# Kernel optimization log

Hardware: AMD Instinct MI355X
Metric: run time of the kernel (lower is better)

The kernel has to match this reference:

```python
import jax, jax.numpy as jnp
import numpy as np

K = 16
NS = [2048, 512, 128]

def _knn(q, r, k):
    # q: [B,M,3] query centers, r: [B,N,3] reference points -> (idx [B,M,k], sqdist [B,M,k])
    d2 = (jnp.sum(q * q, -1)[:, :, None] + jnp.sum(r * r, -1)[:, None, :]
          - 2.0 * jnp.einsum('bmd,bnd->bmn', q, r))
    neg, idx = jax.lax.top_k(-d2, k)
    return idx, jnp.maximum(-neg, 0.0)

def _gather(feat, idx):
    # feat [B,N,C], idx [B,M,k] -> [B,M,k,C]
    return jax.vmap(lambda f, i: f[i])(feat, idx)

def _down(x, pos, n, W1, b1, W2, b2):
    # PointNet++-style TransitionDown: sample n centers, kNN group, rel-pos concat, shared MLP, max-pool
    centers = pos[:, :n]
    idx, _ = _knn(centers, pos, K)
    rel = _gather(pos, idx) - centers[:, :, None, :]           # [B,n,K,3]
    feat = jnp.concatenate([rel, _gather(x, idx)], -1)          # [B,n,K,C+3]
    h = jax.nn.relu(feat @ W1 + b1) @ W2 + b2                   # last_act=False
    return jnp.max(h, axis=2), centers

def _up(xc, pc, prv_feat, prv_pos, W, b):
    # TransitionUp: 3-NN inverse-distance interpolation + skip concat + pointwise conv1d
    idx, d2 = _knn(prv_pos, pc, 3)
    w = 1.0 / (d2 + 1e-8)
    w = w / jnp.sum(w, -1, keepdims=True)
    interp = jnp.sum(_gather(xc, idx) * w[..., None], axis=2)   # [B,Nprv,Cc]
    cat = jnp.concatenate([interp, prv_feat], -1)
    return jax.nn.relu(cat @ W + b)

def setup_inputs() -> dict:
    key = jax.random.key(0)
    ks = jax.random.split(key, 16)
    p = lambda k, s: jax.random.normal(k, s, jnp.float32) * 0.02
    B, N = 4, 8192
    return {
        'x': jax.random.normal(ks[0], (B, N, 3), jnp.float32),
        'pos': jax.random.uniform(ks[1], (B, N, 3), jnp.float32),
        'd0_W1': p(ks[2], (6, 128)),   'd0_b1': jnp.zeros((128,), jnp.float32),
        'd0_W2': p(ks[3], (128, 128)), 'd0_b2': jnp.zeros((128,), jnp.float32),
        'd1_W1': p(ks[4], (131, 256)), 'd1_b1': jnp.zeros((256,), jnp.float32),
        'd1_W2': p(ks[5], (256, 256)), 'd1_b2': jnp.zeros((256,), jnp.float32),
        'd2_W1': p(ks[6], (259, 512)), 'd2_b1': jnp.zeros((512,), jnp.float32),
        'd2_W2': p(ks[7], (512, 512)), 'd2_b2': jnp.zeros((512,), jnp.float32),
        'u0_W': p(ks[8], (768, 256)),  'u0_b': jnp.zeros((256,), jnp.float32),
        'u1_W': p(ks[9], (384, 128)),  'u1_b': jnp.zeros((128,), jnp.float32),
        'u2_W': p(ks[10], (134, 128)), 'u2_b': jnp.zeros((128,), jnp.float32),
        'f_W1': p(ks[11], (128, 128)), 'f_b1': jnp.zeros((128,), jnp.float32),
        'f_W2': p(ks[12], (128, 128)), 'f_b2': jnp.zeros((128,), jnp.float32),
    }

def reference(x, pos, d0_W1, d0_b1, d0_W2, d0_b2, d1_W1, d1_b1, d1_W2, d1_b2,
              d2_W1, d2_b1, d2_W2, d2_b2, u0_W, u0_b, u1_W, u1_b, u2_W, u2_b,
              f_W1, f_b1, f_W2, f_b2):
    pos0, x0 = pos, x
    # encoder (transition-down) with cached (pos, x) per scale
    x1, pos1 = _down(x0, pos0, NS[0], d0_W1, d0_b1, d0_W2, d0_b2)
    x2, pos2 = _down(x1, pos1, NS[1], d1_W1, d1_b1, d1_W2, d1_b2)
    x3, pos3 = _down(x2, pos2, NS[2], d2_W1, d2_b1, d2_W2, d2_b2)
    # decoder (transition-up) consuming the cache in reverse; last level concats raw pos to skip feat
    up = _up(x3, pos3, x2, pos2, u0_W, u0_b)
    up = _up(up, pos2, x1, pos1, u1_W, u1_b)
    prv0 = jnp.concatenate([x0, pos0], -1)
    up = _up(up, pos1, prv0, pos0, u2_W, u2_b)
    # feat_map_layer_out: two pointwise conv1d layers, last_act=False
    out = jax.nn.relu(up @ f_W1 + f_b1) @ f_W2 + f_b2
    return (out, pos0)
```

## Files before the change

kernel.cpp:

```cpp
#include <hip/hip_runtime.h>

#define NFULL 8192
#define BATCH 4

typedef unsigned long long u64;
typedef unsigned int u32;
typedef __attribute__((ext_vector_type(8))) short bf8_t;
typedef __attribute__((ext_vector_type(4))) float f4_t;

__device__ __forceinline__ u32 fbias(float f) {
  u32 u = __float_as_uint(f);
  return (u & 0x80000000u) ? ~u : (u | 0x80000000u);
}
__device__ __forceinline__ float funbias(u32 b) {
  u32 u = (b & 0x80000000u) ? (b & 0x7fffffffu) : ~b;
  return __uint_as_float(u);
}
__device__ __forceinline__ short f2bf(float f) {
  u32 u = __float_as_uint(f);
  u32 r = u + 0x7FFFu + ((u >> 16) & 1u);
  return (short)(r >> 16);
}

__global__ __launch_bounds__(256) void build_grids_kernel(
    const float* __restrict__ pos, float4* __restrict__ sortedA,
    int* __restrict__ csA, float4* __restrict__ sortedB, int* __restrict__ csB,
    float4* __restrict__ sortedC, int* __restrict__ csC) {
  __shared__ int cnt[4096];
  __shared__ int partial[256];
  int which = blockIdx.y, b = blockIdx.x, t = threadIdx.x;
  int NREF = (which == 0) ? 8192 : (which == 1) ? 2048 : 512;
  int GR = (which == 0) ? 16 : 8;
  int NC = GR * GR * GR;
  float4* sorted = ((which == 0) ? sortedA : (which == 1) ? sortedB : sortedC)
                   + (size_t)b * NREF;
  int* cs = ((which == 0) ? csA + b * 4097 : (which == 1) ? csB + b * 513
                                           : csC + b * 513);
  const float* pb = pos + (size_t)b * NFULL * 3;
  for (int c = t; c < NC; c += 256) cnt[c] = 0;
  __syncthreads();
  for (int p = t; p < NREF; p += 256) {
    float x = pb[p * 3 + 0], y = pb[p * 3 + 1], z = pb[p * 3 + 2];
    int cx = min(max((int)(x * GR), 0), GR - 1);
    int cy = min(max((int)(y * GR), 0), GR - 1);
    int cz = min(max((int)(z * GR), 0), GR - 1);
    atomicAdd(&cnt[(cz * GR + cy) * GR + cx], 1);
  }
  __syncthreads();
  int chunk = (NC + 255) / 256;
  int s = 0;
  for (int i = 0; i < chunk; ++i) {
    int c = t * chunk + i;
    if (c < NC) s += cnt[c];
  }
  partial[t] = s;
  __syncthreads();
  if (t == 0) {
    int run = 0;
    for (int i = 0; i < 256; ++i) { int v = partial[i]; partial[i] = run; run += v; }
  }
  __syncthreads();
  int run = partial[t];
  for (int i = 0; i < chunk; ++i) {
    int c = t * chunk + i;
    if (c < NC) { int v = cnt[c]; cnt[c] = run; run += v; }
  }
  __syncthreads();
  for (int c = t; c < NC; c += 256) cs[c] = cnt[c];
  if (t == 0) cs[NC] = NREF;
  __syncthreads();
  for (int p = t; p < NREF; p += 256) {
    float x = pb[p * 3 + 0], y = pb[p * 3 + 1], z = pb[p * 3 + 2];
    int cx = min(max((int)(x * GR), 0), GR - 1);
    int cy = min(max((int)(y * GR), 0), GR - 1);
    int cz = min(max((int)(z * GR), 0), GR - 1);
    int slot = atomicAdd(&cnt[(cz * GR + cy) * GR + cx], 1);
    sorted[slot] = make_float4(x, y, z, __uint_as_float((u32)p));
  }
}

template<int SL>
__device__ __forceinline__ void group_insert(u32 m16, u64 ck, int slot,
                                             u64& val, u64& tau) {
  if (m16) {
    while (m16) {
      int src = __ffs(m16) - 1;
      m16 &= m16 - 1;
      u64 c = __shfl((unsigned long long)ck, src, 16);
      u64 prev = __shfl_up((unsigned long long)val, 1, SL);
      if (slot == 0) prev = 0ull;
      val = (val <= c) ? val : ((prev <= c) ? c : prev);
    }
    tau = __shfl((unsigned long long)val, SL - 1, SL);
  }
}

template<int SL>
__device__ __forceinline__ void first_round_sort(u64 ck, int gl,
                                                 u64& val, u64& tau) {
  u64 v = ck;
#pragma unroll
  for (int size = 2; size <= 16; size <<= 1) {
#pragma unroll
    for (int stride = size >> 1; stride > 0; stride >>= 1) {
      u64 other = __shfl_xor((unsigned long long)v, stride, 16);
      bool ddd = ((gl & size) == 0);
      bool takeMin = (((gl & stride) == 0) == ddd);
      u64 mn = (v <= other) ? v : other;
      u64 mx = (v <= other) ? other : v;
      v = takeMin ? mn : mx;
    }
  }
  if (SL < 16) v = __shfl((unsigned long long)v, gl & (SL - 1), 16);
  val = v;
  tau = __shfl((unsigned long long)v, SL - 1, SL);
}

template<int SL>
__device__ __forceinline__ void scan_range(const float4* __restrict__ sb,
    int s, int e, float qx, float qy, float qz, float qq,
    int g, int gl, int slot, u64& val, u64& tau) {
  for (int t0 = s; t0 < e; t0 += 16) {
    int j = t0 + gl;
    u64 ck = ~0ull;
    if (j < e) {
      float4 P = sb[j];
      float rr = P.x * P.x + P.y * P.y + P.z * P.z;
      float d2 = qq + rr - 2.0f * (qx * P.x + qy * P.y + qz * P.z);
      ck = ((u64)fbias(d2) << 32) | (u32)__float_as_uint(P.w);
    }
    u64 full = __ballot(ck < tau);
    u32 m16 = (u32)((full >> (g * 16)) & 0xFFFFull);
    group_insert<SL>(m16, ck, slot, val, tau);
  }
}


template<int SL, int KOUT, int GR, int R, int NREF>
__device__ __forceinline__ void knn_tail(
    const float4* __restrict__ sb, const int* __restrict__ cs,
    float qx, float qy, float qz, float qq,
    int ix, int iy, int iz, int x0, int x1, int y0, int y1, int z0, int z1,
    int g, int gl, int slot, u64& val, u64& tau) {
  const float h = 1.0f / GR;
  float m = 1e30f;
  if (x0 > 0)      m = fminf(m, qx - x0 * h);
  if (x1 < GR - 1) m = fminf(m, (x1 + 1) * h - qx);
  if (y0 > 0)      m = fminf(m, qy - y0 * h);
  if (y1 < GR - 1) m = fminf(m, (y1 + 1) * h - qy);
  if (z0 > 0)      m = fminf(m, qz - z0 * h);
  if (z1 < GR - 1) m = fminf(m, (z1 + 1) * h - qz);
  float bound = m * m;
  u64 kv = __shfl((unsigned long long)val, KOUT - 1, SL);
  float kth_d2 = funbias((u32)(kv >> 32));
  if (!(kth_d2 < bound)) {
    int X0 = max(ix - (R + 1), 0), X1 = min(ix + (R + 1), GR - 1);
    int Y0 = max(iy - (R + 1), 0), Y1 = min(iy + (R + 1), GR - 1);
    int Z0 = max(iz - (R + 1), 0), Z1 = min(iz + (R + 1), GR - 1);
    int NY2 = Y1 - Y0 + 1;
    int nrow2 = (Z1 - Z0 + 1) * NY2;
    for (int rr2 = 0; rr2 < nrow2; ++rr2) {
      int zz = Z0 + rr2 / NY2, yy = Y0 + rr2 % NY2;
      int c0 = (zz * GR + yy) * GR;
      bool mid = (zz >= z0 && zz <= z1 && yy >= y0 && yy <= y1);
      int s1 = cs[c0 + X0];
      int e1 = mid ? cs[c0 + x0] : cs[c0 + X1 + 1];
      scan_range<SL>(sb, s1, e1, qx, qy, qz, qq, g, gl, slot, val, tau);
      if (mid) {
        int s2 = cs[c0 + x1 + 1];
        int e2 = cs[c0 + X1 + 1];
        scan_range<SL>(sb, s2, e2, qx, qy, qz, qq, g, gl, slot, val, tau);
      }
    }
    x0 = X0; x1 = X1; y0 = Y0; y1 = Y1; z0 = Z0; z1 = Z1;
    m = 1e30f;
    if (x0 > 0)      m = fminf(m, qx - x0 * h);
    if (x1 < GR - 1) m = fminf(m, (x1 + 1) * h - qx);
    if (y0 > 0)      m = fminf(m, qy - y0 * h);
    if (y1 < GR - 1) m = fminf(m, (y1 + 1) * h - qy);
    if (z0 > 0)      m = fminf(m, qz - z0 * h);
    if (z1 < GR - 1) m = fminf(m, (z1 + 1) * h - qz);
    bound = m * m;
    kv = __shfl((unsigned long long)val, KOUT - 1, SL);
    kth_d2 = funbias((u32)(kv >> 32));
    if (!(kth_d2 < bound)) {
      for (int t0 = 0; t0 < NREF; t0 += 16) {
        int j = t0 + gl;
        u64 ck = ~0ull;
        if (j < NREF) {
          float4 P = sb[j];
          int cx = min(max((int)(P.x * GR), 0), GR - 1);
          int cy = min(max((int)(P.y * GR), 0), GR - 1);
          int cz = min(max((int)(P.z * GR), 0), GR - 1);
          bool inbox = (cx >= x0 && cx <= x1 && cy >= y0 && cy <= y1 &&
                        cz >= z0 && cz <= z1);
          if (!inbox) {
            float rr = P.x * P.x + P.y * P.y + P.z * P.z;
            float d2 = qq + rr - 2.0f * (qx * P.x + qy * P.y + qz * P.z);
            ck = ((u64)fbias(d2) << 32) | (u32)__float_as_uint(P.w);
          }
        }
        u64 full = __ballot(ck < tau);
        u32 m16 = (u32)((full >> (g * 16)) & 0xFFFFull);
        group_insert<SL>(m16, ck, slot, val, tau);
      }
    }
  }
}

template<int SL, int KOUT, int GR, int R, int NREF>
__device__ void knn_grid_flat_dev(int vbx,
    const float* __restrict__ pos, const float4* __restrict__ sorted,
    const int* __restrict__ cellStart, int csStride, int Mq,
    int* __restrict__ oidx, float* __restrict__ od2) {
  int b = blockIdx.y;
  int wv = threadIdx.x >> 6, lane = threadIdx.x & 63;
  int g = lane >> 4, gl = lane & 15;
  int q = vbx * 16 + wv * 4 + g;
  const float* pb = pos + (size_t)b * NFULL * 3;
  const float4* sb = sorted + (size_t)b * NREF;
  const int* cs = cellStart + b * csStride;
  float qx = pb[q * 3 + 0], qy = pb[q * 3 + 1], qz = pb[q * 3 + 2];
  float qq = qx * qx + qy * qy + qz * qz;
  int ix = min(max((int)(qx * GR), 0), GR - 1);
  int iy = min(max((int)(qy * GR), 0), GR - 1);
  int iz = min(max((int)(qz * GR), 0), GR - 1);
  int x0 = max(ix - R, 0), x1 = min(ix + R, GR - 1);
  int y0 = max(iy - R, 0), y1 = min(iy + R, GR - 1);
  int z0 = max(iz - R, 0), z1 = min(iz + R, GR - 1);

  int ny = y1 - y0 + 1;
  int nrow = (z1 - z0 + 1) * ny;
  int s_i = 0, len_i = 0;
  if (gl < nrow) {
    int zz = z0 + gl / ny, yy = y0 + gl % ny;
    int c0 = (zz * GR + yy) * GR + x0;
    s_i = cs[c0];
    len_i = cs[c0 + (x1 - x0) + 1] - s_i;
  }
  int p_i = len_i;
#pragma unroll
  for (int st = 1; st < 16; st <<= 1) {
    int o = __shfl_up(p_i, st, 16);
    if (gl >= st) p_i += o;
  }
  int T = __shfl(p_i, 15, 16);
  p_i -= len_i;
  int d_i = s_i - p_i;
  if (gl >= nrow) p_i = 0x7fffffff;

  int slot = gl & (SL - 1);
  u64 val, tau;

  {
    int v = gl;
    int r = 0;
#pragma unroll
    for (int st = 8; st >= 1; st >>= 1) {
      int pc = __shfl(p_i, r + st, 16);
      if (v >= pc) r += st;
    }
    int addr = v + __shfl(d_i, r, 16);
    u64 ck = ~0ull;
    if (v < T) {
      float4 P = sb[addr];
      float rr = P.x * P.x + P.y * P.y + P.z * P.z;
      float d2 = qq + rr - 2.0f * (qx * P.x + qy * P.y + qz * P.z);
      ck = ((u64)fbias(d2) << 32) | (u32)__float_as_uint(P.w);
    }
    first_round_sort<SL>(ck, gl, val, tau);
  }

  for (int v0 = 16; v0 < T; v0 += 16) {
    int v = v0 + gl;
    int r = 0;
#pragma unroll
    for (int st = 8; st >= 1; st >>= 1) {
      int pc = __shfl(p_i, r + st, 16);
      if (v >= pc) r += st;
    }
    int addr = v + __shfl(d_i, r, 16);
    u64 ck = ~0ull;
    if (v < T) {
      float4 P = sb[addr];
      float rr = P.x * P.x + P.y * P.y + P.z * P.z;
      float d2 = qq + rr - 2.0f * (qx * P.x + qy * P.y + qz * P.z);
      ck = ((u64)fbias(d2) << 32) | (u32)__float_as_uint(P.w);
    }
    u64 full = __ballot(ck < tau);
    u32 m16 = (u32)((full >> (g * 16)) & 0xFFFFull);
    group_insert<SL>(m16, ck, slot, val, tau);
  }

  knn_tail<SL, KOUT, GR, R, NREF>(sb, cs, qx, qy, qz, qq,
      ix, iy, iz, x0, x1, y0, y1, z0, z1, g, gl, slot, val, tau);

  if (gl < KOUT) {
    size_t base = ((size_t)b * Mq + q) * KOUT;
    oidx[base + gl] = (int)(u32)val;
    if (od2) od2[base + gl] = fmaxf(funbias((u32)(val >> 32)), 0.0f);
  }
}

template<int SL, int KOUT, int GR, int R, int NREF>
__device__ void knn_grid_flat32_dev(int vbx,
    const float* __restrict__ pos, const float4* __restrict__ sorted,
    const int* __restrict__ cellStart, int csStride, int Mq,
    int* __restrict__ oidx, float* __restrict__ od2) {
  int b = blockIdx.y;
  int wv = threadIdx.x >> 6, lane = threadIdx.x & 63;
  int g = lane >> 4, gl = lane & 15;
  int q = vbx * 16 + wv * 4 + g;
  const float* pb = pos + (size_t)b * NFULL * 3;
  const float4* sb = sorted + (size_t)b * NREF;
  const int* cs = cellStart + b * csStride;
  float qx = pb[q * 3 + 0], qy = pb[q * 3 + 1], qz = pb[q * 3 + 2];
  float qq = qx * qx + qy * qy + qz * qz;
  int ix = min(max((int)(qx * GR), 0), GR - 1);
  int iy = min(max((int)(qy * GR), 0), GR - 1);
  int iz = min(max((int)(qz * GR), 0), GR - 1);
  int x0 = max(ix - R, 0), x1 = min(ix + R, GR - 1);
  int y0 = max(iy - R, 0), y1 = min(iy + R, GR - 1);
  int z0 = max(iz - R, 0), z1 = min(iz + R, GR - 1);

  int ny = y1 - y0 + 1;
  int nrow = (z1 - z0 + 1) * ny;
  int sLo = 0, lenLo = 0, sHi = 0, lenHi = 0;
  if (gl < nrow) {
    int zz = z0 + gl / ny, yy = y0 + gl % ny;
    int c0 = (zz * GR + yy) * GR + x0;
    sLo = cs[c0]; lenLo = cs[c0 + (x1 - x0) + 1] - sLo;
  }
  {
    int i2 = gl + 16;
    if (i2 < nrow) {
      int zz = z0 + i2 / ny, yy = y0 + i2 % ny;
      int c0 = (zz * GR + yy) * GR + x0;
      sHi = cs[c0]; lenHi = cs[c0 + (x1 - x0) + 1] - sHi;
    }
  }
  int pLo = lenLo, pHi = lenHi;
#pragma unroll
  for (int st = 1; st < 16; st <<= 1) {
    int o = __shfl_up(pLo, st, 16);
    if (gl >= st) pLo += o;
    int o2 = __shfl_up(pHi, st, 16);
    if (gl >= st) pHi += o2;
  }
  int tot16 = __shfl(pLo, 15, 16);
  pHi += tot16;
  int T = __shfl(pHi, 15, 16);
  pLo -= lenLo; pHi -= lenHi;
  int dLo = sLo - pLo, dHi = sHi - pHi;
  if (gl >= nrow) pLo = 0x7fffffff;
  if (gl + 16 >= nrow) pHi = 0x7fffffff;

  int slot = gl & (SL - 1);
  u64 val, tau;

  {
    int v = gl;
    int r = 0;
#pragma unroll
    for (int st = 16; st >= 1; st >>= 1) {
      int j = r + st;
      int pcL = __shfl(pLo, j & 15, 16);
      int pcH = __shfl(pHi, j & 15, 16);
      int pc = (j < 16) ? pcL : pcH;
      if (v >= pc) r = j;
    }
    int dL = __shfl(dLo, r & 15, 16);
    int dH = __shfl(dHi, r & 15, 16);
    int addr = v + ((r < 16) ? dL : dH);
    u64 ck = ~0ull;
    if (v < T) {
      float4 P = sb[addr];
      float rr = P.x * P.x + P.y * P.y + P.z * P.z;
      float d2 = qq + rr - 2.0f * (qx * P.x + qy * P.y + qz * P.z);
      ck = ((u64)fbias(d2) << 32) | (u32)__float_as_uint(P.w);
    }
    first_round_sort<SL>(ck, gl, val, tau);
  }

  for (int v0 = 16; v0 < T; v0 += 16) {
    int v = v0 + gl;
    int r = 0;
#pragma unroll
    for (int st = 16; st >= 1; st >>= 1) {
      int j = r + st;
      int pcL = __shfl(pLo, j & 15, 16);
      int pcH = __shfl(pHi, j & 15, 16);
      int pc = (j < 16) ? pcL : pcH;
      if (v >= pc) r = j;
    }
    int dL = __shfl(dLo, r & 15, 16);
    int dH = __shfl(dHi, r & 15, 16);
    int addr = v + ((r < 16) ? dL : dH);
    u64 ck = ~0ull;
    if (v < T) {
      float4 P = sb[addr];
      float rr = P.x * P.x + P.y * P.y + P.z * P.z;
      float d2 = qq + rr - 2.0f * (qx * P.x + qy * P.y + qz * P.z);
      ck = ((u64)fbias(d2) << 32) | (u32)__float_as_uint(P.w);
    }
    u64 full = __ballot(ck < tau);
    u32 m16 = (u32)((full >> (g * 16)) & 0xFFFFull);
    group_insert<SL>(m16, ck, slot, val, tau);
  }

  knn_tail<SL, KOUT, GR, R, NREF>(sb, cs, qx, qy, qz, qq,
      ix, iy, iz, x0, x1, y0, y1, z0, z1, g, gl, slot, val, tau);

  if (gl < KOUT) {
    size_t base = ((size_t)b * Mq + q) * KOUT;
    oidx[base + gl] = (int)(u32)val;
    if (od2) od2[base + gl] = fmaxf(funbias((u32)(val >> 32)), 0.0f);
  }
}

template<int SL, int KOUT>
__device__ void knn_brute_dev(int vbx,
    const float* __restrict__ pos, int Nref, int Mq,
    int* __restrict__ oidx, float* __restrict__ od2) {
  int b = blockIdx.y;
  int wv = threadIdx.x >> 6, lane = threadIdx.x & 63;
  int g = lane >> 4, gl = lane & 15;
  int q = vbx * 16 + wv * 4 + g;
  const float* pb = pos + (size_t)b * NFULL * 3;
  float qx = pb[q * 3 + 0], qy = pb[q * 3 + 1], qz = pb[q * 3 + 2];
  float qq = qx * qx + qy * qy + qz * qz;

  int slot = gl & (SL - 1);
  u64 val, tau;

  {
    int j = gl;
    float rx = pb[j * 3 + 0];
    float ry = pb[j * 3 + 1];
    float rz = pb[j * 3 + 2];
    float rr = rx * rx + ry * ry + rz * rz;
    float d2 = qq + rr - 2.0f * (qx * rx + qy * ry + qz * rz);
    u64 ck = ((u64)fbias(d2) << 32) | (u32)j;
    first_round_sort<SL>(ck, gl, val, tau);
  }

  for (int t0 = 16; t0 < Nref; t0 += 16) {
    int j = t0 + gl;
    float rx = pb[j * 3 + 0];
    float ry = pb[j * 3 + 1];
    float rz = pb[j * 3 + 2];
    float rr = rx * rx + ry * ry + rz * rz;
    float d2 = qq + rr - 2.0f * (qx * rx + qy * ry + qz * rz);
    u64 ck = ((u64)fbias(d2) << 32) | (u32)j;
    u64 full = __ballot(ck < tau);
    u32 m16 = (u32)((full >> (g * 16)) & 0xFFFFull);
    group_insert<SL>(m16, ck, slot, val, tau);
  }

  if (gl < KOUT) {
    size_t base = ((size_t)b * Mq + q) * KOUT;
    oidx[base + gl] = (int)(u32)val;
    if (od2) od2[base + gl] = fmaxf(funbias((u32)(val >> 32)), 0.0f);
  }
}

__global__ __launch_bounds__(256) void knn_all_kernel(
    const float* __restrict__ pos,
    const float4* __restrict__ sortedA, const int* __restrict__ csA,
    const float4* __restrict__ sortedB, const int* __restrict__ csB,
    const float4* __restrict__ sortedC, const int* __restrict__ csC,
    int* __restrict__ idx0, int* __restrict__ idx1, int* __restrict__ idx2,
    int* __restrict__ idxu0, float* __restrict__ d2u0,
    int* __restrict__ idxu1, float* __restrict__ d2u1,
    int* __restrict__ idxu2, float* __restrict__ d2u2) {
  int bx = blockIdx.x;
  if (bx < 8)
    knn_brute_dev<16, 16>(bx, pos, 512, 128, idx2, nullptr);
  else if (bx < 40)
    knn_grid_flat32_dev<16, 16, 8, 2, 2048>(bx - 8, pos, sortedB, csB, 513, 512, idx1, nullptr);
  else if (bx < 168)
    knn_grid_flat32_dev<16, 16, 16, 2, 8192>(bx - 40, pos, sortedA, csA, 4097, 2048, idx0, nullptr);
  else if (bx < 296)
    knn_grid_flat32_dev<4, 3, 8, 2, 512>(bx - 168, pos, sortedC, csC, 513, 2048, idxu1, d2u1);
  else if (bx < 808)
    knn_grid_flat_dev<4, 3, 8, 1, 2048>(bx - 296, pos, sortedB, csB, 513, 8192, idxu2, d2u2);
  else
    knn_brute_dev<4, 3>(bx - 808, pos, 128, 512, idxu0, d2u0);
}

__device__ __forceinline__ void pack_tile_rt(const float* __restrict__ W,
                                             short* __restrict__ outp,
                                             int KDIM, int N, int tile, int lane) {
  int NT = N >> 4;
  int kt = tile / NT, nt = tile - kt * NT;
  int n = nt * 16 + (lane & 15);
  int k0 = kt * 32 + (lane >> 4) * 8;
  bf8_t v;
#pragma unroll
  for (int j = 0; j < 8; ++j) {
    int k = k0 + j;
    v[j] = (k < KDIM) ? f2bf(W[(size_t)k * N + n]) : (short)0;
  }
  *(bf8_t*)(outp + ((size_t)tile * 64 + lane) * 8) = v;
}

__global__ __launch_bounds__(64) void pack_copy_all_kernel(
    const float* d0W1, short* d0W1p, const float* d0W2, short* d0W2p,
    const float* d1W1, short* d1W1p, const float* d1W2, short* d1W2p,
    const float* d2W1, short* d2W1p, const float* d2W2, short* d2W2p,
    const float* u2W, short* u2Wp, const float* fW1, short* fW1p,
    const float* fW2, short* fW2p,
    const float* u0W, short* u0Wp, const float* u1W, short* u1Wp,
    const float* pos, float* posOut) {
  int blk = blockIdx.x, lane = threadIdx.x;
  if      (blk < 8)    pack_tile_rt(d0W1, d0W1p, 6, 128, blk, lane);
  else if (blk < 40)   pack_tile_rt(d0W2, d0W2p, 128, 128, blk - 8, lane);
  else if (blk < 120)  pack_tile_rt(d1W1, d1W1p, 131, 256, blk - 40, lane);
  else if (blk < 248)  pack_tile_rt(d1W2, d1W2p, 256, 256, blk - 120, lane);
  else if (blk < 536)  pack_tile_rt(d2W1, d2W1p, 259, 512, blk - 248, lane);
  else if (blk < 1048) pack_tile_rt(d2W2, d2W2p, 512, 512, blk - 536, lane);
  else if (blk < 1088) pack_tile_rt(u2W, u2Wp, 134, 128, blk - 1048, lane);
  else if (blk < 1120) pack_tile_rt(fW1, fW1p, 128, 128, blk - 1088, lane);
  else if (blk < 1152) pack_tile_rt(fW2, fW2p, 128, 128, blk - 1120, lane);
  else if (blk < 1536) pack_tile_rt(u0W, u0Wp, 768, 256, blk - 1152, lane);
  else if (blk < 1632) pack_tile_rt(u1W, u1Wp, 384, 128, blk - 1536, lane);
  else {
    int base = (blk - 1632) * 256;
#pragma unroll
    for (int j = 0; j < 4; ++j) {
      int i = base + lane + j * 64;
      posOut[i] = pos[i];
    }
  }
}

template<int FEAT, int CIN, int CHID, int FPAD, int QB, int WAVES>
__global__ __launch_bounds__(64 * WAVES) void down_mfma_kernel(
    const float* __restrict__ pos, const float* __restrict__ xin,
    const int* __restrict__ idx,
    const short* __restrict__ W1p, const float* __restrict__ b1,
    const short* __restrict__ W2p, const float* __restrict__ b2,
    float* __restrict__ out, int n, int nprev) {
  const int KT1 = FPAD / 32, NT1 = CHID / 16;
  const int KT2 = CHID / 32, NT2 = CHID / 16;
  __shared__ short sFeat[QB][16][FPAD + 8];
  __shared__ short sH1[QB][16][CHID + 8];
  __shared__ int sIdx[QB][16];
  __shared__ float sCtr[QB][3];
  int b = blockIdx.y, q0 = blockIdx.x * QB;
  int t = threadIdx.x;
  int lane = t & 63, wv = t >> 6;
  const float* pb = pos + (size_t)b * NFULL * 3;
  const float* xb = xin + (size_t)b * nprev * CIN;
  if (t < QB * 16)
    sIdx[t >> 4][t & 15] = idx[((size_t)b * n + q0 + (t >> 4)) * 16 + (t & 15)];
  if (t < QB * 3) sCtr[t / 3][t % 3] = pb[(q0 + t / 3) * 3 + (t % 3)];
  __syncthreads();
  for (int e = t; e < QB * 16 * FPAD; e += 64 * WAVES) {
    int k = e / FPAD, c = e - k * FPAD;
    int qq = k >> 4, kk = k & 15;
    float v = 0.f;
    if (c < 3) v = pb[sIdx[qq][kk] * 3 + c] - sCtr[qq][c];
    else if (c < FEAT) v = xb[(size_t)sIdx[qq][kk] * CIN + (c - 3)];
    sFeat[qq][kk][c] = f2bf(v);
  }
  __syncthreads();

  int col = lane & 15, quad = lane >> 4;
  const bf8_t* W1t = (const bf8_t*)W1p;
  for (int nt = 2 * wv; nt < NT1; nt += 2 * WAVES) {
    f4_t acc[QB][2];
    float bb0 = b1[nt * 16 + col], bb1 = b1[nt * 16 + 16 + col];
#pragma unroll
    for (int q = 0; q < QB; ++q) {
      acc[q][0] = {bb0, bb0, bb0, bb0};
      acc[q][1] = {bb1, bb1, bb1, bb1};
    }
#pragma unroll
    for (int kt = 0; kt < KT1; ++kt) {
      bf8_t bf0 = W1t[(kt * NT1 + nt) * 64 + lane];
      bf8_t bf1 = W1t[(kt * NT1 + nt + 1) * 64 + lane];
#pragma unroll
      for (int q = 0; q < QB; ++q) {
        bf8_t a = *(const bf8_t*)&sFeat[q][col][kt * 32 + quad * 8];
        acc[q][0] = __builtin_amdgcn_mfma_f32_16x16x32_bf16(a, bf0, acc[q][0], 0, 0, 0);
        acc[q][1] = __builtin_amdgcn_mfma_f32_16x16x32_bf16(a, bf1, acc[q][1], 0, 0, 0);
      }
    }
#pragma unroll
    for (int q = 0; q < QB; ++q)
#pragma unroll
      for (int r = 0; r < 4; ++r) {
        sH1[q][quad * 4 + r][nt * 16 + col] = f2bf(fmaxf(acc[q][0][r], 0.f));
        sH1[q][quad * 4 + r][nt * 16 + 16 + col] = f2bf(fmaxf(acc[q][1][r], 0.f));
      }
  }
  __syncthreads();

  const bf8_t* W2t = (const bf8_t*)W2p;
  for (int nt = 2 * wv; nt < NT2; nt += 2 * WAVES) {
    f4_t acc[QB][2];
    float bb0 = b2[nt * 16 + col], bb1 = b2[nt * 16 + 16 + col];
#pragma unroll
    for (int q = 0; q < QB; ++q) {
      acc[q][0] = {bb0, bb0, bb0, bb0};
      acc[q][1] = {bb1, bb1, bb1, bb1};
    }
#pragma unroll
    for (int kt = 0; kt < KT2; ++kt) {
      bf8_t bf0 = W2t[(kt * NT2 + nt) * 64 + lane];
      bf8_t bf1 = W2t[(kt * NT2 + nt + 1) * 64 + lane];
#pragma unroll
      for (int q = 0; q < QB; ++q) {
        bf8_t a = *(const bf8_t*)&sH1[q][col][kt * 32 + quad * 8];
        acc[q][0] = __builtin_amdgcn_mfma_f32_16x16x32_bf16(a, bf0, acc[q][0], 0, 0, 0);
        acc[q][1] = __builtin_amdgcn_mfma_f32_16x16x32_bf16(a, bf1, acc[q][1], 0, 0, 0);
      }
    }
#pragma unroll
    for (int q = 0; q < QB; ++q) {
      float m0 = fmaxf(fmaxf(acc[q][0][0], acc[q][0][1]), fmaxf(acc[q][0][2], acc[q][0][3]));
      float m1 = fmaxf(fmaxf(acc[q][1][0], acc[q][1][1]), fmaxf(acc[q][1][2], acc[q][1][3]));
      m0 = fmaxf(m0, __shfl_xor(m0, 16, 64));
      m0 = fmaxf(m0, __shfl_xor(m0, 32, 64));
      m1 = fmaxf(m1, __shfl_xor(m1, 16, 64));
      m1 = fmaxf(m1, __shfl_xor(m1, 32, 64));
      if (lane < 16) {
        float* ob = out + ((size_t)b * n + q0 + q) * CHID;
        ob[nt * 16 + lane] = m0;
        ob[nt * 16 + 16 + lane] = m1;
      }
    }
  }
}

template<int CIN, int CPRV, int COUT, int WPB>
__global__ __launch_bounds__(64 * WPB) void up_mfma_kernel(
    const float* __restrict__ xc, int ncoarse,
    const int* __restrict__ idx3, const float* __restrict__ d23,
    const float* __restrict__ prv, const short* __restrict__ Wp,
    const float* __restrict__ bvec, float* __restrict__ out, int m) {
  const int CTOT = CIN + CPRV;
  const int KT = CTOT / 32, NT = COUT / 16;
  __shared__ short sA[16][CTOT + 8];
  __shared__ float sWt[16][3];
  __shared__ int   sIt[16][3];
  int b = blockIdx.y, q0 = blockIdx.x * 16, t = threadIdx.x;
  int lane = t & 63, wv = t >> 6;
  if (t < 16) {
    size_t base = ((size_t)b * m + q0 + t) * 3;
    float d0 = d23[base + 0], d1 = d23[base + 1], d2v = d23[base + 2];
    float w0 = 1.f / (d0 + 1e-8f), w1 = 1.f / (d1 + 1e-8f), w2 = 1.f / (d2v + 1e-8f);
    float s = w0 + w1 + w2;
    sWt[t][0] = w0 / s; sWt[t][1] = w1 / s; sWt[t][2] = w2 / s;
    sIt[t][0] = idx3[base + 0]; sIt[t][1] = idx3[base + 1]; sIt[t][2] = idx3[base + 2];
  }
  __syncthreads();
  const float* xb = xc + (size_t)b * ncoarse * CIN;
  const float* pvb = prv + ((size_t)b * m + q0) * CPRV;
  for (int e = t; e < 16 * CIN; e += 64 * WPB) {
    int p = e / CIN, c = e % CIN;
    float v = sWt[p][0] * xb[(size_t)sIt[p][0] * CIN + c]
            + sWt[p][1] * xb[(size_t)sIt[p][1] * CIN + c]
            + sWt[p][2] * xb[(size_t)sIt[p][2] * CIN + c];
    sA[p][c] = f2bf(v);
  }
  for (int e = t; e < 16 * CPRV; e += 64 * WPB) {
    int p = e / CPRV, c = e % CPRV;
    sA[p][CIN + c] = f2bf(pvb[(size_t)p * CPRV + c]);
  }
  __syncthreads();
  int col = lane & 15, quad = lane >> 4;
  const bf8_t* Wt = (const bf8_t*)Wp;
  float* ob = out + ((size_t)b * m + q0) * COUT;
  for (int nt = 2 * wv; nt < NT; nt += 2 * WPB) {
    float bb0 = bvec[nt * 16 + col], bb1 = bvec[nt * 16 + 16 + col];
    f4_t acc0 = {bb0, bb0, bb0, bb0}, acc1 = {bb1, bb1, bb1, bb1};
#pragma unroll
    for (int kt = 0; kt < KT; ++kt) {
      bf8_t a = *(const bf8_t*)&sA[col][kt * 32 + quad * 8];
      bf8_t bf0 = Wt[(kt * NT + nt) * 64 + lane];
      bf8_t bf1 = Wt[(kt * NT + nt + 1) * 64 + lane];
      acc0 = __builtin_amdgcn_mfma_f32_16x16x32_bf16(a, bf0, acc0, 0, 0, 0);
      acc1 = __builtin_amdgcn_mfma_f32_16x16x32_bf16(a, bf1, acc1, 0, 0, 0);
    }
#pragma unroll
    for (int r = 0; r < 4; ++r) {
      ob[(size_t)(quad * 4 + r) * COUT + nt * 16 + col] = fmaxf(acc0[r], 0.f);
      ob[(size_t)(quad * 4 + r) * COUT + nt * 16 + 16 + col] = fmaxf(acc1[r], 0.f);
    }
  }
}

__global__ __launch_bounds__(128) void up2f_mfma_kernel(
    const float* __restrict__ xc,
    const int* __restrict__ idx3, const float* __restrict__ d23,
    const float* __restrict__ x0, const float* __restrict__ pos0,
    const short* __restrict__ u2Wp, const float* __restrict__ u2b,
    const short* __restrict__ fW1p, const float* __restrict__ fb1,
    const short* __restrict__ fW2p, const float* __restrict__ fb2,
    float* __restrict__ out) {
  __shared__ short sA[16][168];
  __shared__ short sB[16][136];
  __shared__ float sWt[16][3];
  __shared__ int   sIt[16][3];
  int b = blockIdx.y, q0 = blockIdx.x * 16, t = threadIdx.x;
  int lane = t & 63, wv = t >> 6;
  if (t < 16) {
    size_t base = ((size_t)b * NFULL + q0 + t) * 3;
    float d0 = d23[base + 0], d1 = d23[base + 1], d2v = d23[base + 2];
    float w0 = 1.f / (d0 + 1e-8f), w1 = 1.f / (d1 + 1e-8f), w2 = 1.f / (d2v + 1e-8f);
    float s = w0 + w1 + w2;
    sWt[t][0] = w0 / s; sWt[t][1] = w1 / s; sWt[t][2] = w2 / s;
    sIt[t][0] = idx3[base + 0]; sIt[t][1] = idx3[base + 1]; sIt[t][2] = idx3[base + 2];
  }
  __syncthreads();
  const float* xb = xc + (size_t)b * 2048 * 128;
#pragma unroll
  for (int p = 0; p < 16; ++p) {
    float v = sWt[p][0] * xb[(size_t)sIt[p][0] * 128 + t]
            + sWt[p][1] * xb[(size_t)sIt[p][1] * 128 + t]
            + sWt[p][2] * xb[(size_t)sIt[p][2] * 128 + t];
    sA[p][t] = f2bf(v);
  }
  for (int e = t; e < 16 * 32; e += 128) {
    int p = e / 32, c = 128 + (e % 32);
    float v = 0.f;
    if (c < 131) v = x0[((size_t)b * NFULL + q0 + p) * 3 + (c - 128)];
    else if (c < 134) v = pos0[((size_t)b * NFULL + q0 + p) * 3 + (c - 131)];
    sA[p][c] = f2bf(v);
  }
  __syncthreads();
  int col = lane & 15, quad = lane >> 4;

  bf8_t a1[5];
#pragma unroll
  for (int kt = 0; kt < 5; ++kt)
    a1[kt] = *(const bf8_t*)&sA[col][kt * 32 + quad * 8];
  const bf8_t* W1t = (const bf8_t*)u2Wp;
  for (int nt = 2 * wv; nt < 8; nt += 4) {
    float bb0 = u2b[nt * 16 + col], bb1 = u2b[nt * 16 + 16 + col];
    f4_t acc0 = {bb0, bb0, bb0, bb0}, acc1 = {bb1, bb1, bb1, bb1};
#pragma unroll
    for (int kt = 0; kt < 5; ++kt) {
      bf8_t bf0 = W1t[(kt * 8 + nt) * 64 + lane];
      bf8_t bf1 = W1t[(kt * 8 + nt + 1) * 64 + lane];
      acc0 = __builtin_amdgcn_mfma_f32_16x16x32_bf16(a1[kt], bf0, acc0, 0, 0, 0);
      acc1 = __builtin_amdgcn_mfma_f32_16x16x32_bf16(a1[kt], bf1, acc1, 0, 0, 0);
    }
#pragma unroll
    for (int r = 0; r < 4; ++r) {
      sB[quad * 4 + r][nt * 16 + col] = f2bf(fmaxf(acc0[r], 0.f));
      sB[quad * 4 + r][nt * 16 + 16 + col] = f2bf(fmaxf(acc1[r], 0.f));
    }
  }
  __syncthreads();

  bf8_t a2[4];
#pragma unroll
  for (int kt = 0; kt < 4; ++kt)
    a2[kt] = *(const bf8_t*)&sB[col][kt * 32 + quad * 8];
  const bf8_t* W2t = (const bf8_t*)fW1p;
  for (int nt = 2 * wv; nt < 8; nt += 4) {
    float bb0 = fb1[nt * 16 + col], bb1 = fb1[nt * 16 + 16 + col];
    f4_t acc0 = {bb0, bb0, bb0, bb0}, acc1 = {bb1, bb1, bb1, bb1};
#pragma unroll
    for (int kt = 0; kt < 4; ++kt) {
      bf8_t bf0 = W2t[(kt * 8 + nt) * 64 + lane];
      bf8_t bf1 = W2t[(kt * 8 + nt + 1) * 64 + lane];
      acc0 = __builtin_amdgcn_mfma_f32_16x16x32_bf16(a2[kt], bf0, acc0, 0, 0, 0);
      acc1 = __builtin_amdgcn_mfma_f32_16x16x32_bf16(a2[kt], bf1, acc1, 0, 0, 0);
    }
#pragma unroll
    for (int r = 0; r < 4; ++r) {
      sA[quad * 4 + r][nt * 16 + col] = f2bf(fmaxf(acc0[r], 0.f));
      sA[quad * 4 + r][nt * 16 + 16 + col] = f2bf(fmaxf(acc1[r], 0.f));
    }
  }
  __syncthreads();

  bf8_t a3[4];
#pragma unroll
  for (int kt = 0; kt < 4; ++kt)
    a3[kt] = *(const bf8_t*)&sA[col][kt * 32 + quad * 8];
  const bf8_t* W3t = (const bf8_t*)fW2p;
  float* ob = out + ((size_t)b * NFULL + q0) * 128;
  for (int nt = 2 * wv; nt < 8; nt += 4) {
    float bb0 = fb2[nt * 16 + col], bb1 = fb2[nt * 16 + 16 + col];
    f4_t acc0 = {bb0, bb0, bb0, bb0}, acc1 = {bb1, bb1, bb1, bb1};
#pragma unroll
    for (int kt = 0; kt < 4; ++kt) {
      bf8_t bf0 = W3t[(kt * 8 + nt) * 64 + lane];
      bf8_t bf1 = W3t[(kt * 8 + nt + 1) * 64 + lane];
      acc0 = __builtin_amdgcn_mfma_f32_16x16x32_bf16(a3[kt], bf0, acc0, 0, 0, 0);
      acc1 = __builtin_amdgcn_mfma_f32_16x16x32_bf16(a3[kt], bf1, acc1, 0, 0, 0);
    }
#pragma unroll
    for (int r = 0; r < 4; ++r) {
      ob[(size_t)(quad * 4 + r) * 128 + nt * 16 + col] = acc0[r];
      ob[(size_t)(quad * 4 + r) * 128 + nt * 16 + 16 + col] = acc1[r];
    }
  }
}

extern "C" void kernel_launch(void* const* d_in, const int* in_sizes, int n_in,
                              void* d_out, int out_size, void* d_ws, size_t ws_size,
                              hipStream_t stream) {
  const float* x    = (const float*)d_in[0];
  const float* pos  = (const float*)d_in[1];
  const float* d0W1 = (const float*)d_in[2];
  const float* d0b1 = (const float*)d_in[3];
  const float* d0W2 = (const float*)d_in[4];
  const float* d0b2 = (const float*)d_in[5];
  const float* d1W1 = (const float*)d_in[6];
  const float* d1b1 = (const float*)d_in[7];
  const float* d1W2 = (const float*)d_in[8];
  const float* d1b2 = (const float*)d_in[9];
  const float* d2W1 = (const float*)d_in[10];
  const float* d2b1 = (const float*)d_in[11];
  const float* d2W2 = (const float*)d_in[12];
  const float* d2b2 = (const float*)d_in[13];
  const float* u0W  = (const float*)d_in[14];
  const float* u0b  = (const float*)d_in[15];
  const float* u1W  = (const float*)d_in[16];
  const float* u1b  = (const float*)d_in[17];
  const float* u2W  = (const float*)d_in[18];
  const float* u2b  = (const float*)d_in[19];
  const float* fW1  = (const float*)d_in[20];
  const float* fb1  = (const float*)d_in[21];
  const float* fW2  = (const float*)d_in[22];
  const float* fb2  = (const float*)d_in[23];

  char* ws = (char*)d_ws;
  float* x1    = (float*)(ws + 0);
  float* x2    = (float*)(ws + 4194304);
  float* x3    = (float*)(ws + 6291456);
  float* up0o  = (float*)(ws + 7340032);
  float* up1o  = (float*)(ws + 9437184);
  int*   idx0  = (int*)  (ws + 13631488);
  int*   idx1  = (int*)  (ws + 14155776);
  int*   idx2  = (int*)  (ws + 14286848);
  float4* sortedC = (float4*)(ws + 14319616);
  int*    csC     = (int*)   (ws + 14352384);
  int*   idxu0 = (int*)  (ws + 14843904);
  float* d2u0  = (float*)(ws + 14868480);
  int*   idxu1 = (int*)  (ws + 14893056);
  float* d2u1  = (float*)(ws + 14991360);
  int*   idxu2 = (int*)  (ws + 15089664);
  float* d2u2  = (float*)(ws + 15482880);
  short* d1W1p = (short*)(ws + 15876096);
  short* d1W2p = (short*)(ws + 15958016);
  short* d2W1p = (short*)(ws + 16089088);
  short* d2W2p = (short*)(ws + 16384000);
  short* d0W1p = (short*)(ws + 16908288);
  short* d0W2p = (short*)(ws + 16916480);
  float4* sortedA = (float4*)(ws + 16949248);
  int*    csA     = (int*)   (ws + 17473536);
  float4* sortedB = (float4*)(ws + 17539136);
  int*    csB     = (int*)   (ws + 17670208);
  short* u2Wp  = (short*)(ws + 17697920);
  short* fW1p  = (short*)(ws + 17738880);
  short* fW2p  = (short*)(ws + 17771648);

  float* out = (float*)d_out;
  short* u0Wp = (short*)out;
  short* u1Wp = (short*)(out + 98304);

  pack_copy_all_kernel<<<dim3(2016), 64, 0, stream>>>(
      d0W1, d0W1p, d0W2, d0W2p, d1W1, d1W1p, d1W2, d1W2p,
      d2W1, d2W1p, d2W2, d2W2p, u2W, u2Wp, fW1, fW1p, fW2, fW2p,
      u0W, u0Wp, u1W, u1Wp,
      pos, out + (size_t)BATCH * NFULL * 128);
  build_grids_kernel<<<dim3(BATCH, 3), 256, 0, stream>>>(
      pos, sortedA, csA, sortedB, csB, sortedC, csC);

  knn_all_kernel<<<dim3(840, BATCH), 256, 0, stream>>>(
      pos, sortedA, csA, sortedB, csB, sortedC, csC,
      idx0, idx1, idx2,
      idxu0, d2u0, idxu1, d2u1, idxu2, d2u2);

  down_mfma_kernel<6, 3, 128, 32, 4, 4><<<dim3(512, BATCH), 256, 0, stream>>>(
      pos, x, idx0, d0W1p, d0b1, d0W2p, d0b2, x1, 2048, 8192);
  down_mfma_kernel<131, 128, 256, 160, 4, 8><<<dim3(128, BATCH), 512, 0, stream>>>(
      pos, x1, idx1, d1W1p, d1b1, d1W2p, d1b2, x2, 512, 2048);
  down_mfma_kernel<259, 256, 512, 288, 2, 8><<<dim3(64, BATCH), 512, 0, stream>>>(
      pos, x2, idx2, d2W1p, d2b1, d2W2p, d2b2, x3, 128, 512);

  up_mfma_kernel<512, 256, 256, 4><<<dim3(32, BATCH), 256, 0, stream>>>(
      x3, 128, idxu0, d2u0, x2, u0Wp, u0b, up0o, 512);
  up_mfma_kernel<256, 128, 128, 2><<<dim3(128, BATCH), 128, 0, stream>>>(
      up0o, 512, idxu1, d2u1, x1, u1Wp, u1b, up1o, 2048);
  up2f_mfma_kernel<<<dim3(512, BATCH), 128, 0, stream>>>(
      up1o, idxu2, d2u2, x, pos, u2Wp, u2b, fW1p, fb1, fW2p, fb2, out);
}
```

Baseline: 306.1 us.

## Use per-lane top-3 registers with a final cross-lane merge for 3-NN searches

For the three 3-NN interpolation searches, each of the 16 lanes per query now keeps its own sorted top-3 in registers and inserts candidates with compare-swaps. The shared-threshold ballot plus group insertion is gone, and a shuffle-min merge runs only before the bound checks and at the end. This removes per-candidate cross-lane ballots and shuffles in the hot scan loop. The cost is that no shared pruning threshold exists during the scan, and a merge is needed at each tail-expansion decision.

```diff
diff --git a/kernel.cpp b/kernel.cpp
--- a/kernel.cpp
+++ b/kernel.cpp
@@ -114,6 +114,50 @@
   if (SL < 16) v = __shfl((unsigned long long)v, gl & (SL - 1), 16);
   val = v;
   tau = __shfl((unsigned long long)v, SL - 1, SL);
+}
+
+__device__ __forceinline__ void lane_insert3(u64 ck, u64& v0, u64& v1, u64& v2) {
+  u64 a = (v0 <= ck) ? v0 : ck;
+  u64 bb = (v0 <= ck) ? ck : v0;
+  v0 = a;
+  u64 c = (v1 <= bb) ? v1 : bb;
+  u64 d = (v1 <= bb) ? bb : v1;
+  v1 = c;
+  v2 = (v2 <= d) ? v2 : d;
+}
+
+__device__ __forceinline__ void merge3(u64 v0, u64 v1, u64 v2,
+                                       u64& o0, u64& o1, u64& o2) {
+  u64 h = v0;
+  int hc = 0;
+  u64 outs[3];
+#pragma unroll
+  for (int k = 0; k < 3; ++k) {
+    u64 m = h;
+#pragma unroll
+    for (int st = 1; st < 16; st <<= 1) {
+      u64 o = __shfl_xor((unsigned long long)m, st, 16);
+      m = (m <= o) ? m : o;
+    }
+    outs[k] = m;
+    if (h == m) { ++hc; h = (hc == 1) ? v1 : ((hc == 2) ? v2 : ~0ull); }
+  }
+  o0 = outs[0]; o1 = outs[1]; o2 = outs[2];
+}
+
+__device__ __forceinline__ void scan_range3(const float4* __restrict__ sb,
+    int s, int e, float qx, float qy, float qz, float qq,
+    int gl, u64& v0, u64& v1, u64& v2) {
+  for (int t0 = s; t0 < e; t0 += 16) {
+    int j = t0 + gl;
+    if (j < e) {
+      float4 P = sb[j];
+      float rr = P.x * P.x + P.y * P.y + P.z * P.z;
+      float d2 = qq + rr - 2.0f * (qx * P.x + qy * P.y + qz * P.z);
+      u64 ck = ((u64)fbias(d2) << 32) | (u32)__float_as_uint(P.w);
+      lane_insert3(ck, v0, v1, v2);
+    }
+  }
 }
 
 template<int SL>
@@ -208,8 +252,78 @@
   }
 }
 
-template<int SL, int KOUT, int GR, int R, int NREF>
-__device__ void knn_grid_flat_dev(int vbx,
+template<int GR, int R, int NREF>
+__device__ __forceinline__ void knn_tail3(
+    const float4* __restrict__ sb, const int* __restrict__ cs,
+    float qx, float qy, float qz, float qq,
+    int ix, int iy, int iz, int x0, int x1, int y0, int y1, int z0, int z1,
+    int gl, u64& v0, u64& v1, u64& v2, u64& o0, u64& o1, u64& o2) {
+  const float h = 1.0f / GR;
+  float m = 1e30f;
+  if (x0 > 0)      m = fminf(m, qx - x0 * h);
+  if (x1 < GR - 1) m = fminf(m, (x1 + 1) * h - qx);
+  if (y0 > 0)      m = fminf(m, qy - y0 * h);
+  if (y1 < GR - 1) m = fminf(m, (y1 + 1) * h - qy);
+  if (z0 > 0)      m = fminf(m, qz - z0 * h);
+  if (z1 < GR - 1) m = fminf(m, (z1 + 1) * h - qz);
+  float bound = m * m;
+  merge3(v0, v1, v2, o0, o1, o2);
+  float kth_d2 = funbias((u32)(o2 >> 32));
+  if (!(kth_d2 < bound)) {
+    int X0 = max(ix - (R + 1), 0), X1 = min(ix + (R + 1), GR - 1);
+    int Y0 = max(iy - (R + 1), 0), Y1 = min(iy + (R + 1), GR - 1);
+    int Z0 = max(iz - (R + 1), 0), Z1 = min(iz + (R + 1), GR - 1);
+    int NY2 = Y1 - Y0 + 1;
+    int nrow2 = (Z1 - Z0 + 1) * NY2;
+    for (int rr2 = 0; rr2 < nrow2; ++rr2) {
+      int zz = Z0 + rr2 / NY2, yy = Y0 + rr2 % NY2;
+      int c0 = (zz * GR + yy) * GR;
+      bool mid = (zz >= z0 && zz <= z1 && yy >= y0 && yy <= y1);
+      int s1 = cs[c0 + X0];
+      int e1 = mid ? cs[c0 + x0] : cs[c0 + X1 + 1];
+      scan_range3(sb, s1, e1, qx, qy, qz, qq, gl, v0, v1, v2);
+      if (mid) {
+        int s2 = cs[c0 + x1 + 1];
+        int e2 = cs[c0 + X1 + 1];
+        scan_range3(sb, s2, e2, qx, qy, qz, qq, gl, v0, v1, v2);
+      }
+    }
+    x0 = X0; x1 = X1; y0 = Y0; y1 = Y1; z0 = Z0; z1 = Z1;
+    m = 1e30f;
+    if (x0 > 0)      m = fminf(m, qx - x0 * h);
+    if (x1 < GR - 1) m = fminf(m, (x1 + 1) * h - qx);
+    if (y0 > 0)      m = fminf(m, qy - y0 * h);
+    if (y1 < GR - 1) m = fminf(m, (y1 + 1) * h - qy);
+    if (z0 > 0)      m = fminf(m, qz - z0 * h);
+    if (z1 < GR - 1) m = fminf(m, (z1 + 1) * h - qz);
+    bound = m * m;
+    merge3(v0, v1, v2, o0, o1, o2);
+    kth_d2 = funbias((u32)(o2 >> 32));
+    if (!(kth_d2 < bound)) {
+      for (int t0 = 0; t0 < NREF; t0 += 16) {
+        int j = t0 + gl;
+        if (j < NREF) {
+          float4 P = sb[j];
+          int cx = min(max((int)(P.x * GR), 0), GR - 1);
+          int cy = min(max((int)(P.y * GR), 0), GR - 1);
+          int cz = min(max((int)(P.z * GR), 0), GR - 1);
+          bool inbox = (cx >= x0 && cx <= x1 && cy >= y0 && cy <= y1 &&
+                        cz >= z0 && cz <= z1);
+          if (!inbox) {
+            float rr = P.x * P.x + P.y * P.y + P.z * P.z;
+            float d2 = qq + rr - 2.0f * (qx * P.x + qy * P.y + qz * P.z);
+            u64 ck = ((u64)fbias(d2) << 32) | (u32)__float_as_uint(P.w);
+            lane_insert3(ck, v0, v1, v2);
+          }
+        }
+      }
+      merge3(v0, v1, v2, o0, o1, o2);
+    }
+  }
+}
+
+template<int GR, int R, int NREF>
+__device__ void knn_grid_flat3_dev(int vbx,
     const float* __restrict__ pos, const float4* __restrict__ sorted,
     const int* __restrict__ cellStart, int csStride, int Mq,
     int* __restrict__ oidx, float* __restrict__ od2) {
@@ -249,11 +363,10 @@
   int d_i = s_i - p_i;
   if (gl >= nrow) p_i = 0x7fffffff;
 
-  int slot = gl & (SL - 1);
-  u64 val, tau;
-
-  {
-    int v = gl;
+  u64 v0 = ~0ull, v1 = ~0ull, v2 = ~0ull;
+
+  for (int vb = 0; vb < T; vb += 16) {
+    int v = vb + gl;
     int r = 0;
 #pragma unroll
     for (int st = 8; st >= 1; st >>= 1) {
@@ -261,44 +374,146 @@
       if (v >= pc) r += st;
     }
     int addr = v + __shfl(d_i, r, 16);
-    u64 ck = ~0ull;
     if (v < T) {
       float4 P = sb[addr];
       float rr = P.x * P.x + P.y * P.y + P.z * P.z;
       float d2 = qq + rr - 2.0f * (qx * P.x + qy * P.y + qz * P.z);
-      ck = ((u64)fbias(d2) << 32) | (u32)__float_as_uint(P.w);
-    }
-    first_round_sort<SL>(ck, gl, val, tau);
-  }
-
-  for (int v0 = 16; v0 < T; v0 += 16) {
-    int v = v0 + gl;
+      u64 ck = ((u64)fbias(d2) << 32) | (u32)__float_as_uint(P.w);
+      lane_insert3(ck, v0, v1, v2);
+    }
+  }
+
+  u64 o0, o1, o2;
+  knn_tail3<GR, R, NREF>(sb, cs, qx, qy, qz, qq,
+      ix, iy, iz, x0, x1, y0, y1, z0, z1, gl, v0, v1, v2, o0, o1, o2);
+
+  if (gl < 3) {
+    u64 val = (gl == 0) ? o0 : ((gl == 1) ? o1 : o2);
+    size_t base = ((size_t)b * Mq + q) * 3;
+    oidx[base + gl] = (int)(u32)val;
+    od2[base + gl] = fmaxf(funbias((u32)(val >> 32)), 0.0f);
+  }
+}
+
+template<int GR, int R, int NREF>
+__device__ void knn_grid_flat32_3_dev(int vbx,
+    const float* __restrict__ pos, const float4* __restrict__ sorted,
+    const int* __restrict__ cellStart, int csStride, int Mq,
+    int* __restrict__ oidx, float* __restrict__ od2) {
+  int b = blockIdx.y;
+  int wv = threadIdx.x >> 6, lane = threadIdx.x & 63;
+  int g = lane >> 4, gl = lane & 15;
+  int q = vbx * 16 + wv * 4 + g;
+  const float* pb = pos + (size_t)b * NFULL * 3;
+  const float4* sb = sorted + (size_t)b * NREF;
+  const int* cs = cellStart + b * csStride;
+  float qx = pb[q * 3 + 0], qy = pb[q * 3 + 1], qz = pb[q * 3 + 2];
+  float qq = qx * qx + qy * qy + qz * qz;
+  int ix = min(max((int)(qx * GR), 0), GR - 1);
+  int iy = min(max((int)(qy * GR), 0), GR - 1);
+  int iz = min(max((int)(qz * GR), 0), GR - 1);
+  int x0 = max(ix - R, 0), x1 = min(ix + R, GR - 1);
+  int y0 = max(iy - R, 0), y1 = min(iy + R, GR - 1);
+  int z0 = max(iz - R, 0), z1 = min(iz + R, GR - 1);
+
+  int ny = y1 - y0 + 1;
+  int nrow = (z1 - z0 + 1) * ny;
+  int sLo = 0, lenLo = 0, sHi = 0, lenHi = 0;
+  if (gl < nrow) {
+    int zz = z0 + gl / ny, yy = y0 + gl % ny;
+    int c0 = (zz * GR + yy) * GR + x0;
+    sLo = cs[c0]; lenLo = cs[c0 + (x1 - x0) + 1] - sLo;
+  }
+  {
+    int i2 = gl + 16;
+    if (i2 < nrow) {
+      int zz = z0 + i2 / ny, yy = y0 + i2 % ny;
+      int c0 = (zz * GR + yy) * GR + x0;
+      sHi = cs[c0]; lenHi = cs[c0 + (x1 - x0) + 1] - sHi;
+    }
+  }
+  int pLo = lenLo, pHi = lenHi;
+#pragma unroll
+  for (int st = 1; st < 16; st <<= 1) {
+    int o = __shfl_up(pLo, st, 16);
+    if (gl >= st) pLo += o;
+    int o2_ = __shfl_up(pHi, st, 16);
+    if (gl >= st) pHi += o2_;
+  }
+  int tot16 = __shfl(pLo, 15, 16);
+  pHi += tot16;
+  int T = __shfl(pHi, 15, 16);
+  pLo -= lenLo; pHi -= lenHi;
+  int dLo = sLo - pLo, dHi = sHi - pHi;
+  if (gl >= nrow) pLo = 0x7fffffff;
+  if (gl + 16 >= nrow) pHi = 0x7fffffff;
+
+  u64 v0 = ~0ull, v1 = ~0ull, v2 = ~0ull;
+
+  for (int vb = 0; vb < T; vb += 16) {
+    int v = vb + gl;
     int r = 0;
 #pragma unroll
-    for (int st = 8; st >= 1; st >>= 1) {
-      int pc = __shfl(p_i, r + st, 16);
-      if (v >= pc) r += st;
-    }
-    int addr = v + __shfl(d_i, r, 16);
-    u64 ck = ~0ull;
+    for (int st = 16; st >= 1; st >>= 1) {
+      int j = r + st;
+      int pcL = __shfl(pLo, j & 15, 16);
+      int pcH = __shfl(pHi, j & 15, 16);
+      int pc = (j < 16) ? pcL : pcH;
+      if (v >= pc) r = j;
+    }
+    int dL = __shfl(dLo, r & 15, 16);
+    int dH = __shfl(dHi, r & 15, 16);
+    int addr = v + ((r < 16) ? dL : dH);
     if (v < T) {
       float4 P = sb[addr];
       float rr = P.x * P.x + P.y * P.y + P.z * P.z;
       float d2 = qq + rr - 2.0f * (qx * P.x + qy * P.y + qz * P.z);
-      ck = ((u64)fbias(d2) << 32) | (u32)__float_as_uint(P.w);
-    }
-    u64 full = __ballot(ck < tau);
-    u32 m16 = (u32)((full >> (g * 16)) & 0xFFFFull);
-    group_insert<SL>(m16, ck, slot, val, tau);
-  }
-
-  knn_tail<SL, KOUT, GR, R, NREF>(sb, cs, qx, qy, qz, qq,
-      ix, iy, iz, x0, x1, y0, y1, z0, z1, g, gl, slot, val, tau);
-
-  if (gl < KOUT) {
-    size_t base = ((size_t)b * Mq + q) * KOUT;
+      u64 ck = ((u64)fbias(d2) << 32) | (u32)__float_as_uint(P.w);
+      lane_insert3(ck, v0, v1, v2);
+    }
+  }
+
+  u64 o0, o1, o2;
+  knn_tail3<GR, R, NREF>(sb, cs, qx, qy, qz, qq,
+      ix, iy, iz, x0, x1, y0, y1, z0, z1, gl, v0, v1, v2, o0, o1, o2);
+
+  if (gl < 3) {
+    u64 val = (gl == 0) ? o0 : ((gl == 1) ? o1 : o2);
+    size_t base = ((size_t)b * Mq + q) * 3;
     oidx[base + gl] = (int)(u32)val;
-    if (od2) od2[base + gl] = fmaxf(funbias((u32)(val >> 32)), 0.0f);
+    od2[base + gl] = fmaxf(funbias((u32)(val >> 32)), 0.0f);
+  }
+}
+
+__device__ void knn_brute3_dev(int vbx,
+    const float* __restrict__ pos, int Nref, int Mq,
+    int* __restrict__ oidx, float* __restrict__ od2) {
+  int b = blockIdx.y;
+  int wv = threadIdx.x >> 6, lane = threadIdx.x & 63;
+  int g = lane >> 4, gl = lane & 15;
+  int q = vbx * 16 + wv * 4 + g;
+  const float* pb = pos + (size_t)b * NFULL * 3;
+  float qx = pb[q * 3 + 0], qy = pb[q * 3 + 1], qz = pb[q * 3 + 2];
+  float qq = qx * qx + qy * qy + qz * qz;
+
+  u64 v0 = ~0ull, v1 = ~0ull, v2 = ~0ull;
+  for (int j = gl; j < Nref; j += 16) {
+    float rx = pb[j * 3 + 0];
+    float ry = pb[j * 3 + 1];
+    float rz = pb[j * 3 + 2];
+    float rr = rx * rx + ry * ry + rz * rz;
+    float d2 = qq + rr - 2.0f * (qx * rx + qy * ry + qz * rz);
+    u64 ck = ((u64)fbias(d2) << 32) | (u32)j;
+    lane_insert3(ck, v0, v1, v2);
+  }
+  u64 o0, o1, o2;
+  merge3(v0, v1, v2, o0, o1, o2);
+
+  if (gl < 3) {
+    u64 val = (gl == 0) ? o0 : ((gl == 1) ? o1 : o2);
+    size_t base = ((size_t)b * Mq + q) * 3;
+    oidx[base + gl] = (int)(u32)val;
+    od2[base + gl] = fmaxf(funbias((u32)(val >> 32)), 0.0f);
   }
 }
 
@@ -481,11 +696,11 @@
   else if (bx < 168)
     knn_grid_flat32_dev<16, 16, 16, 2, 8192>(bx - 40, pos, sortedA, csA, 4097, 2048, idx0, nullptr);
   else if (bx < 296)
-    knn_grid_flat32_dev<4, 3, 8, 2, 512>(bx - 168, pos, sortedC, csC, 513, 2048, idxu1, d2u1);
+    knn_grid_flat32_3_dev<8, 2, 512>(bx - 168, pos, sortedC, csC, 513, 2048, idxu1, d2u1);
   else if (bx < 808)
-    knn_grid_flat_dev<4, 3, 8, 1, 2048>(bx - 296, pos, sortedB, csB, 513, 8192, idxu2, d2u2);
+    knn_grid_flat3_dev<8, 1, 2048>(bx - 296, pos, sortedB, csB, 513, 8192, idxu2, d2u2);
   else
-    knn_brute_dev<4, 3>(bx - 808, pos, 128, 512, idxu0, d2u0);
+    knn_brute3_dev(bx - 808, pos, 128, 512, idxu0, d2u0);
 }
 
 __device__ __forceinline__ void pack_tile_rt(const float* __restrict__ W,
```

Result: faster. 299.9 us (-2.1%).
